# Kernel tuning notes

Measured on AMD Instinct MI355X. Metric: run time of the kernel, lower is better.

## Reference

```python
import jax, jax.numpy as jnp
import numpy as np

B, L, D = 2, 2048, 1024
H, K = 16, 16
HD = D // H


def setup_inputs() -> dict:
    key = jax.random.key(0)
    k1, k2, k3, k4, k5 = jax.random.split(key, 5)
    x = jax.random.normal(k1, (B, L, D), dtype=jnp.float32)
    # Linear weight (out_features, in_features), small init to keep logits sane
    w_in = jax.random.normal(k2, (3 * D, D), dtype=jnp.float32) * 0.02
    # TISA radial-basis kernel parameters, per (head, kernel)
    kernel_offsets = jax.random.normal(k3, (H, K), dtype=jnp.float32) * 20.0
    kernel_amplitudes = 0.1 + 0.01 * jax.random.normal(k4, (H, K), dtype=jnp.float32)
    kernel_sharpness = 0.1 + 0.01 * jax.random.normal(k5, (H, K), dtype=jnp.float32)
    return {"x": x, "w_in": w_in, "kernel_offsets": kernel_offsets,
            "kernel_amplitudes": kernel_amplitudes, "kernel_sharpness": kernel_sharpness}


def tisa_bias(offsets, amplitudes, sharpness, seq_len):
    # relative positions -(L-1) .. (L-1)  -> per-head RBF positional scores
    rel = jnp.arange(-(seq_len - 1), seq_len, dtype=jnp.float32)  # (2L-1,)
    # scores[h, m] = sum_k amp[h,k] * exp(-|sharp[h,k]| * (off[h,k] - rel[m])^2)
    diff = offsets[:, :, None] - rel[None, None, :]               # (H, K, 2L-1)
    scores = jnp.sum(amplitudes[:, :, None] * jnp.exp(-jnp.abs(sharpness)[:, :, None] * diff * diff), axis=1)  # (H, 2L-1)
    # Toeplitz expansion: bias[h, i, j] = scores[h, (i - j) + (L-1)]
    i = jnp.arange(seq_len)
    idx = i[:, None] - i[None, :] + (seq_len - 1)                 # (L, L)
    return scores[:, idx]                                         # (H, L, L)


def reference(x, w_in, kernel_offsets, kernel_amplitudes, kernel_sharpness):
    b, l, d = x.shape
    proj = jnp.einsum('bld,ed->ble', x, w_in)                     # (B, L, 3D)
    # split: memory = first 2D (k then v), query = last D
    k_, v_, q_ = proj[..., :d], proj[..., d:2 * d], proj[..., 2 * d:]

    def heads(t):
        return t.reshape(b, l, H, HD).transpose(0, 2, 1, 3)       # (B, H, L, HD)

    q, k, v = heads(q_), heads(k_), heads(v_)
    bias = tisa_bias(kernel_offsets, kernel_amplitudes, kernel_sharpness, l)  # (H, L, L)
    scale = 1.0 / np.sqrt(HD).astype(np.float32)
    logits = jnp.einsum('bhld,bhmd->bhlm', q, k) * scale + bias[None]
    attn = jax.nn.softmax(logits, axis=-1)
    out = jnp.einsum('bhlm,bhmd->bhld', attn, v)                  # (B, H, L, HD)
    return out.transpose(0, 2, 1, 3).reshape(b, l, d)             # (B, L, D)
```

## Files before the change

### kernel.cpp

```cpp
#include <hip/hip_runtime.h>
#include <hip/hip_bf16.h>
#include <stdint.h>
#include <stddef.h>


#define NB     2
#define NH     16
#define SL     2048
#define DH     64
#define DMODEL 1024
#define SCP    4096
#define LOG2E  1.44269504088896340736f

typedef __attribute__((ext_vector_type(8)))  short bf16x8;
typedef __attribute__((ext_vector_type(4)))  short bf16x4;
typedef __attribute__((ext_vector_type(4)))  float f32x4;
typedef __attribute__((ext_vector_type(16))) float f32x16;

static __device__ __forceinline__ short f2bf(float x) {
  __hip_bfloat16 h = __float2bfloat16(x);
  return *reinterpret_cast<short*>(&h);
}
static __device__ __forceinline__ short f2bf_fast(float x) {
  union { float f; uint32_t u; } v; v.f = x;
  return (short)((v.u + 0x8000u) >> 16);
}
static __device__ __forceinline__ long long bf4_to_ll(bf16x4 v) {
  long long r; __builtin_memcpy(&r, &v, 8); return r;
}
static __device__ __forceinline__ bf16x4 ll_to_bf4(long long v) {
  bf16x4 r; __builtin_memcpy(&r, &v, 8); return r;
}
static __device__ __forceinline__ float fexp2(float x) {
#if __has_builtin(__builtin_amdgcn_exp2f)
  return __builtin_amdgcn_exp2f(x);
#else
  return __expf(x * 0.69314718056f);
#endif
}
#define GLD(g, l) __builtin_amdgcn_global_load_lds( \
    (const __attribute__((address_space(1))) void*)(g), \
    (__attribute__((address_space(3))) void*)(l), 16, 0, 0)

__global__ __launch_bounds__(256) void prep_k(
    const float* __restrict__ x, const float* __restrict__ w,
    const float* __restrict__ koff, const float* __restrict__ kamp,
    const float* __restrict__ kshp,
    short* __restrict__ xbf, short* __restrict__ wbf,
    float* __restrict__ scores) {
  const int bx = blockIdx.x, tid = threadIdx.x;
  if (bx < 3584) {
    const float* src = (bx < 2048) ? x : w;
    short* dst       = (bx < 2048) ? xbf : wbf;
    const size_t i   = ((size_t)(bx < 2048 ? bx : bx - 2048) * 256 + tid) * 8;
    float4 a = *(const float4*)(src + i);
    float4 b = *(const float4*)(src + i + 4);
    bf16x8 o;
    o[0] = f2bf(a.x); o[1] = f2bf(a.y); o[2] = f2bf(a.z); o[3] = f2bf(a.w);
    o[4] = f2bf(b.x); o[5] = f2bf(b.y); o[6] = f2bf(b.z); o[7] = f2bf(b.w);
    *(bf16x8*)(dst + i) = o;
  } else {
    const int idx = bx - 3584;
    const int h = idx >> 4;
    const int r = (idx & 15) * 256 + tid;
    if (r >= 4095) return;
    float rel = (float)(r - (SL - 1));
    float acc = 0.f;
#pragma unroll
    for (int k = 0; k < 16; ++k) {
      float o = koff[h * 16 + k];
      float a = kamp[h * 16 + k];
      float s = fabsf(kshp[h * 16 + k]);
      float d = o - rel;
      acc += a * __expf(-s * d * d);
    }
    scores[h * SCP + r] = acc * LOG2E;
  }
}

__global__ __launch_bounds__(256) void qkv_gemm_k(
    const short* __restrict__ A, const short* __restrict__ Bw,
    __hip_bfloat16* __restrict__ kbuf, __hip_bfloat16* __restrict__ vbufT,
    __hip_bfloat16* __restrict__ qbuf) {
  __shared__ __align__(16) short SM[12288];
  short* As = SM;
  short* Bs = SM + 8192;
  const int tid  = threadIdx.x;
  const int lane = tid & 63;
  const int wv   = tid >> 6;
  const int l15  = lane & 15, quad = lane >> 4;
  const int wm = (wv & 1) * 64, wn = (wv >> 1) * 32;
  const int xt = blockIdx.x, yt = blockIdx.y;
  const int m0 = yt * 128, n0 = xt * 64;
  const int which = xt >> 4;
  const int hh    = xt & 15;

  f32x4 acc[4][2];
#pragma unroll
  for (int r = 0; r < 4; ++r)
#pragma unroll
    for (int c = 0; c < 2; ++c) acc[r][c] = (f32x4){0.f, 0.f, 0.f, 0.f};

  for (int kt = 0; kt < 16; ++kt) {
    const int k0 = kt * 64;
#pragma unroll
    for (int it = 0; it < 4; ++it) {
      const int e8  = it * 256 + tid;
      GLD(A + (size_t)(m0 + (e8 >> 3)) * DMODEL + k0 + (e8 & 7) * 8, &As[e8 * 8]);
    }
#pragma unroll
    for (int it = 0; it < 2; ++it) {
      const int e8  = it * 256 + tid;
      GLD(Bw + (size_t)(n0 + (e8 >> 3)) * DMODEL + k0 + (e8 & 7) * 8, &Bs[e8 * 8]);
    }
    __syncthreads();
#pragma unroll
    for (int ki = 0; ki < 64; ki += 32) {
      bf16x8 af[4], bfv[2];
#pragma unroll
      for (int r = 0; r < 4; ++r)
        af[r] = *(const bf16x8*)&As[(wm + r * 16 + l15) * 64 + ki + quad * 8];
#pragma unroll
      for (int c = 0; c < 2; ++c)
        bfv[c] = *(const bf16x8*)&Bs[(wn + c * 16 + l15) * 64 + ki + quad * 8];
#pragma unroll
      for (int r = 0; r < 4; ++r)
#pragma unroll
        for (int c = 0; c < 2; ++c)
          acc[r][c] = __builtin_amdgcn_mfma_f32_16x16x32_bf16(af[r], bfv[c], acc[r][c], 0, 0, 0);
    }
    __syncthreads();
  }

  const int bb  = m0 >> 11;
  const int llb = m0 & 2047;
  if (which != 1) {
    const float qs = (which == 2) ? 0.125f * LOG2E : 1.0f;
#pragma unroll
    for (int r = 0; r < 4; ++r)
#pragma unroll
      for (int c = 0; c < 2; ++c)
#pragma unroll
        for (int gg = 0; gg < 4; ++gg)
          SM[(wm + r * 16 + quad * 4 + gg) * 72 + wn + c * 16 + l15] =
              f2bf_fast(acc[r][c][gg] * qs);
    __syncthreads();
    __hip_bfloat16* dst = (which == 0) ? kbuf : qbuf;
#pragma unroll
    for (int i = 0; i < 4; ++i) {
      const int cidx = i * 256 + tid;
      const int m = cidx >> 3, ch = cidx & 7;
      bf16x8 val = *(const bf16x8*)&SM[m * 72 + ch * 8];
      *(bf16x8*)&dst[(((size_t)bb * NH + hh) * SL + llb + m) * DH + ch * 8] = val;
    }
  } else {
#pragma unroll
    for (int r = 0; r < 4; ++r)
#pragma unroll
      for (int c = 0; c < 2; ++c) {
        bf16x4 pk;
#pragma unroll
        for (int gg = 0; gg < 4; ++gg) pk[gg] = f2bf_fast(acc[r][c][gg]);
        *(bf16x4*)&SM[(wn + c * 16 + l15) * 136 + wm + r * 16 + quad * 4] = pk;
      }
    __syncthreads();
#pragma unroll
    for (int i = 0; i < 4; ++i) {
      const int cidx = i * 256 + tid;
      const int n = cidx >> 4, ch = cidx & 15;
      bf16x8 val = *(const bf16x8*)&SM[n * 136 + ch * 8];
      *(bf16x8*)&vbufT[(((size_t)bb * NH + hh) * DH + n) * SL + llb + ch * 8] = val;
    }
  }
}

__global__ __launch_bounds__(512, 4) void attn_k(
    const __hip_bfloat16* __restrict__ qbuf, const __hip_bfloat16* __restrict__ kbuf,
    const __hip_bfloat16* __restrict__ vbufT, const float* __restrict__ scores,
    float* __restrict__ out) {
  __shared__ __align__(16) short Ks[2][64 * 72];
  __shared__ __align__(16) short Vs[2][64 * 72];
  __shared__ __align__(16) float Bt[2][192];
  const int bh   = blockIdx.x;
  const int b    = bh >> 4, h = bh & 15;
  const int tid  = threadIdx.x;
  const int lane = tid & 63;
  const int w    = tid >> 6;
  const int wv   = w & 3;
  const int kw   = w >> 2;
  const int n32  = lane & 31, hf = lane >> 5;
  const int i0b  = blockIdx.y * 128;
  const int i0   = i0b + wv * 32;
  const __hip_bfloat16* qb = qbuf + (size_t)bh * SL * DH;
  const short* kb = (const short*)(kbuf + (size_t)bh * SL * DH);
  const short* vb = (const short*)(vbufT + (size_t)bh * DH * SL);
  const float* sc = scores + h * SCP;

  bf16x8 qf[4];
#pragma unroll
  for (int kc = 0; kc < 4; ++kc)
    qf[kc] = *(const bf16x8*)&qb[(size_t)(i0 + n32) * DH + kc * 16 + hf * 8];

  f32x16 ot[2];
#pragma unroll
  for (int dt = 0; dt < 2; ++dt)
#pragma unroll
    for (int r = 0; r < 16; ++r) ot[dt][r] = 0.f;
  float ls[4] = {0.f, 0.f, 0.f, 0.f};

  auto stage = [&](int bsel, int j0) {
    const short* ksrc = kb + (size_t)j0 * DH;
    {
      int c = tid; int r = c / 9, s = c - r * 9;
      GLD(ksrc + (size_t)r * DH + s * 8, &Ks[bsel][c * 8]);
    }
    if (tid < 64) {
      int c = 512 + tid; int r = c / 9, s = c - r * 9;
      GLD(ksrc + (size_t)r * DH + s * 8, &Ks[bsel][c * 8]);
    }
    {
      int c = tid; int r = c / 9, s = c - r * 9;
      GLD(vb + (size_t)r * SL + j0 + s * 8, &Vs[bsel][c * 8]);
    }
    if (tid < 64) {
      int c = 512 + tid; int r = c / 9, s = c - r * 9;
      GLD(vb + (size_t)r * SL + j0 + s * 8, &Vs[bsel][c * 8]);
    }
    if (tid < 48) GLD(sc + (i0b - j0 + 1984) + tid * 4, &Bt[bsel][tid * 4]);
  };

  auto compute = [&](int bsel) {
    const short* Kp = Ks[bsel];
    const short* Vp = Vs[bsel];
    const float* Bp = Bt[bsel];
    f32x16 st;
    const int tb0 = wv * 32 + n32 - kw * 32 - 4 * hf + 63;
#pragma unroll
    for (int g = 0; g < 4; ++g)
#pragma unroll
      for (int i = 0; i < 4; ++i) st[g * 4 + i] = Bp[tb0 - 8 * g - i];
    __builtin_amdgcn_s_setprio(1);
#pragma unroll
    for (int kc = 0; kc < 4; ++kc) {
      bf16x8 kf = *(const bf16x8*)&Kp[(kw * 32 + n32) * 72 + kc * 16 + hf * 8];
      st = __builtin_amdgcn_mfma_f32_32x32x16_bf16(kf, qf[kc], st, 0, 0, 0);
    }
    __builtin_amdgcn_s_setprio(0);
    bf16x4 pk[4];
#pragma unroll
    for (int g = 0; g < 4; ++g)
#pragma unroll
      for (int i = 0; i < 4; ++i) {
        const float p = fexp2(st[g * 4 + i]);
        ls[g] += p;
        pk[g][i] = f2bf_fast(p);
      }
    long long s0 = hf ? bf4_to_ll(pk[0]) : bf4_to_ll(pk[1]);
    bf16x4 r0 = ll_to_bf4(__shfl_xor(s0, 32));
    bf16x8 pf0 = hf == 0 ? __builtin_shufflevector(pk[0], r0, 0, 1, 2, 3, 4, 5, 6, 7)
                         : __builtin_shufflevector(r0, pk[1], 0, 1, 2, 3, 4, 5, 6, 7);
    long long s1 = hf ? bf4_to_ll(pk[2]) : bf4_to_ll(pk[3]);
    bf16x4 r1 = ll_to_bf4(__shfl_xor(s1, 32));
    bf16x8 pf1 = hf == 0 ? __builtin_shufflevector(pk[2], r1, 0, 1, 2, 3, 4, 5, 6, 7)
                         : __builtin_shufflevector(r1, pk[3], 0, 1, 2, 3, 4, 5, 6, 7);
    __builtin_amdgcn_s_setprio(1);
#pragma unroll
    for (int dt = 0; dt < 2; ++dt) {
      const short* vr = &Vp[(dt * 32 + n32) * 72 + kw * 32];
      bf16x8 vf0 = *(const bf16x8*)&vr[hf * 8];
      bf16x8 vf1 = *(const bf16x8*)&vr[16 + hf * 8];
      ot[dt] = __builtin_amdgcn_mfma_f32_32x32x16_bf16(vf0, pf0, ot[dt], 0, 0, 0);
      ot[dt] = __builtin_amdgcn_mfma_f32_32x32x16_bf16(vf1, pf1, ot[dt], 0, 0, 0);
    }
    __builtin_amdgcn_s_setprio(0);
  };

  stage(0, 0);
  __syncthreads();
  int cur = 0;
  for (int j0 = 64; j0 < SL; j0 += 64) {
    stage(cur ^ 1, j0);
    compute(cur);
    __syncthreads();
    cur ^= 1;
  }
  compute(cur);
  __syncthreads();

  float lsum = (ls[0] + ls[1]) + (ls[2] + ls[3]);
  lsum += __shfl_xor(lsum, 32);
  float* red = (wv < 2)
      ? (float*)&Ks[0][0] + ((wv * 64 + lane) * 36)
      : (float*)&Vs[0][0] + (((wv - 2) * 64 + lane) * 36);
  if (kw == 1) {
#pragma unroll
    for (int dt = 0; dt < 2; ++dt)
#pragma unroll
      for (int g = 0; g < 4; ++g) {
        f32x4 v;
#pragma unroll
        for (int i = 0; i < 4; ++i) v[i] = ot[dt][g * 4 + i];
        *(f32x4*)&red[dt * 16 + g * 4] = v;
      }
    red[32] = lsum;
  }
  __syncthreads();
  if (kw == 0) {
#pragma unroll
    for (int dt = 0; dt < 2; ++dt)
#pragma unroll
      for (int g = 0; g < 4; ++g) {
        f32x4 v = *(const f32x4*)&red[dt * 16 + g * 4];
#pragma unroll
        for (int i = 0; i < 4; ++i) ot[dt][g * 4 + i] += v[i];
      }
    lsum += red[32];
    const float inv = 1.f / lsum;
    float* orow = out + (((size_t)b * SL + i0 + n32) * NH + h) * DH;
#pragma unroll
    for (int dt = 0; dt < 2; ++dt)
#pragma unroll
      for (int g = 0; g < 4; ++g) {
        f32x4 v;
#pragma unroll
        for (int i = 0; i < 4; ++i) v[i] = ot[dt][g * 4 + i] * inv;
        *(f32x4*)&orow[dt * 32 + 8 * g + 4 * hf] = v;
      }
  }
}

extern "C" void kernel_launch(void* const* d_in, const int* in_sizes, int n_in,
                              void* d_out, int out_size, void* d_ws, size_t ws_size,
                              hipStream_t stream) {
  const float* x    = (const float*)d_in[0];
  const float* w    = (const float*)d_in[1];
  const float* koff = (const float*)d_in[2];
  const float* kamp = (const float*)d_in[3];
  const float* kshp = (const float*)d_in[4];
  float* out = (float*)d_out;

  const size_t per = (size_t)NB * NH * SL * DH;
  const size_t nx  = (size_t)NB * SL * DMODEL;
  const size_t nw  = (size_t)3 * DMODEL * DMODEL;

  __hip_bfloat16* kbuf  = (__hip_bfloat16*)d_ws;
  __hip_bfloat16* vbufT = kbuf + per;
  __hip_bfloat16* qbuf  = vbufT + per;
  float* scores = (float*)(qbuf + per);
  short* xbf    = (short*)(scores + (size_t)NH * SCP);
  short* wbf    = xbf + nx;

  prep_k<<<3840, 256, 0, stream>>>(x, w, koff, kamp, kshp, xbf, wbf, scores);
  qkv_gemm_k<<<dim3(48, 32), 256, 0, stream>>>(xbf, wbf, kbuf, vbufT, qbuf);
  attn_k<<<dim3(NB * NH, SL / 128), 512, 0, stream>>>(qbuf, kbuf, vbufT, scores, out);
}
```

Before: 174.4 us.

## Double-buffer QKV GEMM shared-memory tiles with halved K-step

Restructures the QKV projection GEMM main loop into a two-buffer pipeline. The K tile shrinks from 64 to 32 so that two A/B buffers fit in the existing shared array, and the loads for the next tile are issued before computing the current one. This removes one barrier per iteration and is meant to hide global-load latency behind MFMA work. In exchange it doubles the iteration count and gives less MFMA work per barrier, and the 64-byte shared-memory rows may cause bank conflicts.

```diff
diff --git a/kernel.cpp b/kernel.cpp
--- a/kernel.cpp
+++ b/kernel.cpp
@@ -83,8 +83,6 @@
     __hip_bfloat16* __restrict__ kbuf, __hip_bfloat16* __restrict__ vbufT,
     __hip_bfloat16* __restrict__ qbuf) {
   __shared__ __align__(16) short SM[12288];
-  short* As = SM;
-  short* Bs = SM + 8192;
   const int tid  = threadIdx.x;
   const int lane = tid & 63;
   const int wv   = tid >> 6;
@@ -101,36 +99,48 @@
 #pragma unroll
     for (int c = 0; c < 2; ++c) acc[r][c] = (f32x4){0.f, 0.f, 0.f, 0.f};
 
-  for (int kt = 0; kt < 16; ++kt) {
-    const int k0 = kt * 64;
-#pragma unroll
-    for (int it = 0; it < 4; ++it) {
-      const int e8  = it * 256 + tid;
-      GLD(A + (size_t)(m0 + (e8 >> 3)) * DMODEL + k0 + (e8 & 7) * 8, &As[e8 * 8]);
-    }
+  auto stage = [&](int bsel, int k0) {
+    short* As = SM + bsel * 6144;
+    short* Bs = As + 4096;
 #pragma unroll
     for (int it = 0; it < 2; ++it) {
-      const int e8  = it * 256 + tid;
-      GLD(Bw + (size_t)(n0 + (e8 >> 3)) * DMODEL + k0 + (e8 & 7) * 8, &Bs[e8 * 8]);
-    }
+      const int e8 = it * 256 + tid;
+      GLD(A + (size_t)(m0 + (e8 >> 2)) * DMODEL + k0 + (e8 & 3) * 8, &As[e8 * 8]);
+    }
+    {
+      const int e8 = tid;
+      GLD(Bw + (size_t)(n0 + (e8 >> 2)) * DMODEL + k0 + (e8 & 3) * 8, &Bs[e8 * 8]);
+    }
+  };
+
+  auto compute = [&](int bsel) {
+    const short* As = SM + bsel * 6144;
+    const short* Bs = As + 4096;
+    bf16x8 af[4], bfv[2];
+#pragma unroll
+    for (int r = 0; r < 4; ++r)
+      af[r] = *(const bf16x8*)&As[(wm + r * 16 + l15) * 32 + quad * 8];
+#pragma unroll
+    for (int c = 0; c < 2; ++c)
+      bfv[c] = *(const bf16x8*)&Bs[(wn + c * 16 + l15) * 32 + quad * 8];
+#pragma unroll
+    for (int r = 0; r < 4; ++r)
+#pragma unroll
+      for (int c = 0; c < 2; ++c)
+        acc[r][c] = __builtin_amdgcn_mfma_f32_16x16x32_bf16(af[r], bfv[c], acc[r][c], 0, 0, 0);
+  };
+
+  stage(0, 0);
+  __syncthreads();
+  int cur = 0;
+  for (int kt = 1; kt < 32; ++kt) {
+    stage(cur ^ 1, kt * 32);
+    compute(cur);
     __syncthreads();
-#pragma unroll
-    for (int ki = 0; ki < 64; ki += 32) {
-      bf16x8 af[4], bfv[2];
-#pragma unroll
-      for (int r = 0; r < 4; ++r)
-        af[r] = *(const bf16x8*)&As[(wm + r * 16 + l15) * 64 + ki + quad * 8];
-#pragma unroll
-      for (int c = 0; c < 2; ++c)
-        bfv[c] = *(const bf16x8*)&Bs[(wn + c * 16 + l15) * 64 + ki + quad * 8];
-#pragma unroll
-      for (int r = 0; r < 4; ++r)
-#pragma unroll
-        for (int c = 0; c < 2; ++c)
-          acc[r][c] = __builtin_amdgcn_mfma_f32_16x16x32_bf16(af[r], bfv[c], acc[r][c], 0, 0, 0);
-    }
-    __syncthreads();
-  }
+    cur ^= 1;
+  }
+  compute(cur);
+  __syncthreads();
 
   const int bb  = m0 >> 11;
   const int llb = m0 & 2047;
```

Measured after the change: 177.7 us. No clear change (+1.9%).
